# Optimization experiments

Measured on AMD Instinct MI355X. Metric: run time of the kernel, lower is better.

The kernel has to match this reference:

```python
import jax, jax.numpy as jnp
import numpy as np

U, N, E, D = 200000, 50000, 1600000, 64


def setup_inputs() -> dict:
    key = jax.random.key(0)
    ks = jax.random.split(key, 8)
    nodes = jax.random.randint(ks[0], (N,), 0, U)
    neigh_idx = jax.random.randint(ks[1], (E,), 0, U)
    seg_ids = jnp.sort(jax.random.randint(ks[2], (E,), 0, N))
    u2e = jax.random.normal(ks[3], (U, D), dtype=jnp.float32) * 0.1
    W1 = jax.random.normal(ks[4], (2 * D, D), dtype=jnp.float32) * 0.1
    b1 = jnp.zeros((D,), dtype=jnp.float32)
    W2 = jax.random.normal(ks[5], (D, D), dtype=jnp.float32) * 0.1
    b2 = jnp.zeros((D,), dtype=jnp.float32)
    w3 = jax.random.normal(ks[6], (D, 1), dtype=jnp.float32) * 0.1
    b3 = jnp.zeros((1,), dtype=jnp.float32)
    return {"nodes": nodes, "neigh_idx": neigh_idx, "seg_ids": seg_ids,
            "u2e": u2e, "W1": W1, "b1": b1, "W2": W2, "b2": b2,
            "w3": w3, "b3": b3}


def reference(nodes, neigh_idx, seg_ids, u2e, W1, b1, W2, b2, w3, b3):
    # Per-node self representation  [N, D]
    u_rep = u2e[nodes]
    # Ragged neighbor gather flattened to edge list
    e_u = u2e[neigh_idx]                      # [E, D]
    u_edge = u_rep[seg_ids]                   # [E, D] node rep broadcast to its edges
    # Attention MLP (GraphRec-style), eval mode (no dropout)
    x = jnp.concatenate([e_u, u_edge], axis=1)            # [E, 2D]
    x = jax.nn.relu(x @ W1 + b1)
    x = jax.nn.relu(x @ W2 + b2)
    logits = (x @ w3 + b3)[:, 0]                           # [E]
    # Segment softmax over each node's neighbor set
    seg_max = jax.ops.segment_max(logits, seg_ids, num_segments=N)
    ex = jnp.exp(logits - seg_max[seg_ids])
    denom = jax.ops.segment_sum(ex, seg_ids, num_segments=N)
    att = ex / denom[seg_ids]                              # [E]
    # Attention-weighted neighbor aggregation: e_u^T @ att per node
    agg = jax.ops.segment_sum(att[:, None] * e_u, seg_ids, num_segments=N)  # [N, D]
    # Nodes with zero neighbors fall back to their own embedding
    counts = jax.ops.segment_sum(jnp.ones((E,), dtype=jnp.float32), seg_ids, num_segments=N)
    out = jnp.where(counts[:, None] > 0, agg, u_rep)
    return out
```

## Files before the change

kernel.cpp:

```cpp
#include <hip/hip_runtime.h>
#include <math.h>

#define D 64

typedef __fp16 fp16x2 __attribute__((ext_vector_type(2)));
typedef _Float16 half8 __attribute__((ext_vector_type(8)));
typedef __attribute__((ext_vector_type(4))) float f32x4;

union h8pun { half8 v; fp16x2 h2[4]; };

__global__ __launch_bounds__(256) void k_transpose_all(const float* __restrict__ W1,
                                                       const float* __restrict__ W2,
                                                       float* __restrict__ W1at,
                                                       float* __restrict__ W1bt,
                                                       float* __restrict__ W2t) {
    int i = blockIdx.x * 256 + threadIdx.x;
    if (i >= 3 * D * D) return;
    int mat = i / (D * D), j = i % (D * D);
    int r = j >> 6, c = j & 63;
    if (mat == 0)      W1at[c * D + r] = W1[r * D + c];
    else if (mat == 1) W1bt[c * D + r] = W1[(D + r) * D + c];
    else               W2t[c * D + r] = W2[r * D + c];
}

__global__ __launch_bounds__(256) void k_bounds(const int* __restrict__ seg_ids,
                                                int* __restrict__ start, int E, int N) {
    int n = blockIdx.x * 256 + threadIdx.x;
    if (n > N) return;
    int lo = 0, hi = E;
    while (lo < hi) {
        int mid = (lo + hi) >> 1;
        if (seg_ids[mid] < n) lo = mid + 1; else hi = mid;
    }
    start[n] = lo;
}

__global__ __launch_bounds__(256) void k_proj_mfma(const float* __restrict__ u2e,
                                                   const int* __restrict__ idx,
                                                   const float* __restrict__ Wt,
                                                   const float* __restrict__ bias,
                                                   _Float16* __restrict__ outp,
                                                   _Float16* __restrict__ u2e_h,
                                                   int R) {
    int lane = threadIdx.x & 63;
    int m = lane & 15, quad = lane >> 4;

    half8 Bf[2][4];
    float bv[4];
#pragma unroll
    for (int t = 0; t < 4; ++t) {
        int n = m + 16 * t;
        bv[t] = bias ? bias[n] : 0.0f;
#pragma unroll
        for (int kh = 0; kh < 2; ++kh) {
            const float* col = Wt + n * D + kh * 32 + quad * 8;
#pragma unroll
            for (int j = 0; j < 8; ++j) Bf[kh][t][j] = (_Float16)col[j];
        }
    }

    int ngroups = (R + 15) / 16;
    int wave = (blockIdx.x * blockDim.x + threadIdx.x) >> 6;
    int nwaves = (gridDim.x * blockDim.x) >> 6;
    for (int g = wave; g < ngroups; g += nwaves) {
        int r_ = g * 16 + m;
        int rs = r_ < R ? r_ : R - 1;
        int src = idx ? idx[rs] : rs;
        const float4* arow = (const float4*)(u2e + (size_t)src * D);
        float4 x0 = arow[quad * 2], x1 = arow[quad * 2 + 1];
        float4 y0 = arow[8 + quad * 2], y1 = arow[8 + quad * 2 + 1];
        h8pun A0, A1;
        A0.h2[0] = __builtin_amdgcn_cvt_pkrtz(x0.x, x0.y);
        A0.h2[1] = __builtin_amdgcn_cvt_pkrtz(x0.z, x0.w);
        A0.h2[2] = __builtin_amdgcn_cvt_pkrtz(x1.x, x1.y);
        A0.h2[3] = __builtin_amdgcn_cvt_pkrtz(x1.z, x1.w);
        A1.h2[0] = __builtin_amdgcn_cvt_pkrtz(y0.x, y0.y);
        A1.h2[1] = __builtin_amdgcn_cvt_pkrtz(y0.z, y0.w);
        A1.h2[2] = __builtin_amdgcn_cvt_pkrtz(y1.x, y1.y);
        A1.h2[3] = __builtin_amdgcn_cvt_pkrtz(y1.z, y1.w);
        if (u2e_h && r_ < R) {
            *(half8*)(u2e_h + (size_t)r_ * D + quad * 8) = A0.v;
            *(half8*)(u2e_h + (size_t)r_ * D + 32 + quad * 8) = A1.v;
        }
        f32x4 C[4];
#pragma unroll
        for (int t = 0; t < 4; ++t) C[t] = (f32x4){bv[t], bv[t], bv[t], bv[t]};
#pragma unroll
        for (int t = 0; t < 4; ++t) {
            C[t] = __builtin_amdgcn_mfma_f32_16x16x32_f16(A0.v, Bf[0][t], C[t], 0, 0, 0);
            C[t] = __builtin_amdgcn_mfma_f32_16x16x32_f16(A1.v, Bf[1][t], C[t], 0, 0, 0);
        }
#pragma unroll
        for (int r = 0; r < 4; ++r) {
            int row = g * 16 + quad * 4 + r;
            if (row < R) {
#pragma unroll
                for (int t = 0; t < 4; ++t)
                    outp[(size_t)row * D + m + 16 * t] = (_Float16)C[t][r];
            }
        }
    }
}

__global__ __launch_bounds__(256) void k_edge_logits_mfma(const int* __restrict__ neigh_idx,
                                                          const int* __restrict__ seg_ids,
                                                          const _Float16* __restrict__ q,
                                                          const _Float16* __restrict__ p,
                                                          const float* __restrict__ W2t,
                                                          const float* __restrict__ b2,
                                                          const float* __restrict__ w3,
                                                          const float* __restrict__ b3,
                                                          float* __restrict__ logits, int E) {
    int lane = threadIdx.x & 63;
    int m = lane & 15, quad = lane >> 4;

    half8 Bf[2][4];
    float b2v[4], w3v[4];
#pragma unroll
    for (int t = 0; t < 4; ++t) {
        int n = m + 16 * t;
        b2v[t] = b2[n];
        w3v[t] = w3[n];
#pragma unroll
        for (int kh = 0; kh < 2; ++kh) {
            const float* col = W2t + n * D + kh * 32 + quad * 8;
#pragma unroll
            for (int j = 0; j < 8; ++j) Bf[kh][t][j] = (_Float16)col[j];
        }
    }
    float b3v = b3[0];
    const half8 hz = {0, 0, 0, 0, 0, 0, 0, 0};

    int ngroups = (E + 31) / 32;
    int wave = (blockIdx.x * blockDim.x + threadIdx.x) >> 6;
    int nwaves = (gridDim.x * blockDim.x) >> 6;
    for (int g = wave; g < ngroups; g += nwaves) {
        int ea = g * 32 + m, eb = ea + 16;
        int eas = ea < E ? ea : E - 1;
        int ebs = eb < E ? eb : E - 1;
        int nbra = neigh_idx[eas], sega = seg_ids[eas];
        int nbrb = neigh_idx[ebs], segb = seg_ids[ebs];
        const half8* qra = (const half8*)(q + (size_t)nbra * D);
        const half8* pra = (const half8*)(p + (size_t)sega * D);
        const half8* qrb = (const half8*)(q + (size_t)nbrb * D);
        const half8* prb = (const half8*)(p + (size_t)segb * D);
        half8 qa0 = qra[quad], qa1 = qra[quad + 4];
        half8 pa0 = pra[quad], pa1 = pra[quad + 4];
        half8 qb0 = qrb[quad], qb1 = qrb[quad + 4];
        half8 pb0 = prb[quad], pb1 = prb[quad + 4];
        half8 Aa0 = __builtin_elementwise_max(qa0 + pa0, hz);
        half8 Aa1 = __builtin_elementwise_max(qa1 + pa1, hz);
        half8 Ab0 = __builtin_elementwise_max(qb0 + pb0, hz);
        half8 Ab1 = __builtin_elementwise_max(qb1 + pb1, hz);
        f32x4 Ca[4], Cb[4];
#pragma unroll
        for (int t = 0; t < 4; ++t) {
            Ca[t] = (f32x4){b2v[t], b2v[t], b2v[t], b2v[t]};
            Cb[t] = Ca[t];
        }
#pragma unroll
        for (int t = 0; t < 4; ++t) {
            Ca[t] = __builtin_amdgcn_mfma_f32_16x16x32_f16(Aa0, Bf[0][t], Ca[t], 0, 0, 0);
            Ca[t] = __builtin_amdgcn_mfma_f32_16x16x32_f16(Aa1, Bf[1][t], Ca[t], 0, 0, 0);
            Cb[t] = __builtin_amdgcn_mfma_f32_16x16x32_f16(Ab0, Bf[0][t], Cb[t], 0, 0, 0);
            Cb[t] = __builtin_amdgcn_mfma_f32_16x16x32_f16(Ab1, Bf[1][t], Cb[t], 0, 0, 0);
        }
        float pa[4], pb[4];
#pragma unroll
        for (int r = 0; r < 4; ++r) {
            float sa = 0.0f, sb = 0.0f;
#pragma unroll
            for (int t = 0; t < 4; ++t) {
                sa += fmaxf(Ca[t][r], 0.0f) * w3v[t];
                sb += fmaxf(Cb[t][r], 0.0f) * w3v[t];
            }
            pa[r] = sa; pb[r] = sb;
        }
#pragma unroll
        for (int off = 1; off <= 8; off <<= 1) {
#pragma unroll
            for (int r = 0; r < 4; ++r) {
                pa[r] += __shfl_xor(pa[r], off, 64);
                pb[r] += __shfl_xor(pb[r], off, 64);
            }
        }
        if (m == 0) {
            int e0 = g * 32 + quad * 4;
            if (e0 + 3 < E)
                *(float4*)(logits + e0) = make_float4(pa[0] + b3v, pa[1] + b3v, pa[2] + b3v, pa[3] + b3v);
            else
#pragma unroll
                for (int r = 0; r < 4; ++r)
                    if (e0 + r < E) logits[e0 + r] = pa[r] + b3v;
            int e1 = e0 + 16;
            if (e1 + 3 < E)
                *(float4*)(logits + e1) = make_float4(pb[0] + b3v, pb[1] + b3v, pb[2] + b3v, pb[3] + b3v);
            else
#pragma unroll
                for (int r = 0; r < 4; ++r)
                    if (e1 + r < E) logits[e1 + r] = pb[r] + b3v;
        }
    }
}

__global__ __launch_bounds__(256) void k_agg(const int* __restrict__ nodes,
                                             const int* __restrict__ neigh_idx,
                                             const float* __restrict__ u2e,
                                             const _Float16* __restrict__ u2e_h,
                                             const float* __restrict__ logits,
                                             const int* __restrict__ start,
                                             float* __restrict__ out, int N) {
    int n = blockIdx.x * 4 + ((int)threadIdx.x >> 6);
    int lane = threadIdx.x & 63;
    if (n >= N) return;
    int s = start[n];
    int t = start[n + 1];
    if (s == t) {
        int node = nodes[n];
        out[(size_t)n * D + lane] = u2e[(size_t)node * D + lane];
        return;
    }
    float mx = -INFINITY;
    for (int i = s + lane; i < t; i += 64) mx = fmaxf(mx, logits[i]);
#pragma unroll
    for (int off = 32; off >= 1; off >>= 1) mx = fmaxf(mx, __shfl_xor(mx, off, 64));
    float ssum = 0.0f;
    for (int i = s + lane; i < t; i += 64) ssum += __expf(logits[i] - mx);
#pragma unroll
    for (int off = 32; off >= 1; off >>= 1) ssum += __shfl_xor(ssum, off, 64);
    float inv = 1.0f / ssum;

    int grp = lane >> 3, sub = lane & 7;
    float acc[8];
#pragma unroll
    for (int j = 0; j < 8; ++j) acc[j] = 0.0f;
    for (int i = s; i < t; i += 32) {
#pragma unroll
        for (int uu = 0; uu < 4; ++uu) {
            int ii = i + uu * 8 + grp;
            bool v = ii < t;
            int is = v ? ii : s;
            float lg = logits[is];
            int nb = neigh_idx[is];
            half8 r = *(const half8*)(u2e_h + (size_t)nb * D + sub * 8);
            float a = v ? __expf(lg - mx) * inv : 0.0f;
#pragma unroll
            for (int j = 0; j < 8; ++j) acc[j] += a * (float)r[j];
        }
    }
#pragma unroll
    for (int off = 8; off <= 32; off <<= 1) {
#pragma unroll
        for (int j = 0; j < 8; ++j) acc[j] += __shfl_xor(acc[j], off, 64);
    }
    if (grp == 0) {
        float* o = out + (size_t)n * D + sub * 8;
        *(float4*)o = make_float4(acc[0], acc[1], acc[2], acc[3]);
        *(float4*)(o + 4) = make_float4(acc[4], acc[5], acc[6], acc[7]);
    }
}

extern "C" void kernel_launch(void* const* d_in, const int* in_sizes, int n_in,
                              void* d_out, int out_size, void* d_ws, size_t ws_size,
                              hipStream_t stream) {
    const int* nodes = (const int*)d_in[0];
    const int* neigh_idx = (const int*)d_in[1];
    const int* seg_ids = (const int*)d_in[2];
    const float* u2e = (const float*)d_in[3];
    const float* W1 = (const float*)d_in[4];
    const float* b1 = (const float*)d_in[5];
    const float* W2 = (const float*)d_in[6];
    const float* b2 = (const float*)d_in[7];
    const float* w3 = (const float*)d_in[8];
    const float* b3 = (const float*)d_in[9];
    float* out = (float*)d_out;

    int N = in_sizes[0];
    int E = in_sizes[1];
    int U = in_sizes[3] / D;

    char* ws = (char*)d_ws;
    size_t off = 0;
    auto alloc = [&](size_t bytes) {
        void* ptr = ws + off;
        off = (off + bytes + 255) & ~(size_t)255;
        return ptr;
    };
    float* logits = (float*)alloc((size_t)E * 4);
    int* start = (int*)alloc((size_t)(N + 1) * 4);
    float* W1at = (float*)alloc((size_t)D * D * 4);
    float* W1bt = (float*)alloc((size_t)D * D * 4);
    float* W2t = (float*)alloc((size_t)D * D * 4);
    _Float16* q = (_Float16*)alloc((size_t)U * D * 2);
    _Float16* p = (_Float16*)alloc((size_t)N * D * 2);
    _Float16* u2e_h = (_Float16*)alloc((size_t)U * D * 2);
    (void)ws_size;

    k_transpose_all<<<(3 * D * D + 255) / 256, 256, 0, stream>>>(W1, W2, W1at, W1bt, W2t);
    k_bounds<<<(N + 1 + 255) / 256, 256, 0, stream>>>(seg_ids, start, E, N);
    k_proj_mfma<<<1024, 256, 0, stream>>>(u2e, nullptr, W1at, nullptr, q, u2e_h, U);
    k_proj_mfma<<<256, 256, 0, stream>>>(u2e, nodes, W1bt, b1, p, nullptr, N);
    k_edge_logits_mfma<<<2048, 256, 0, stream>>>(neigh_idx, seg_ids, q, p, W2t,
                                                 b2, w3, b3, logits, E);
    k_agg<<<(N + 3) / 4, 256, 0, stream>>>(nodes, neigh_idx, u2e, u2e_h, logits, start, out, N);
}
```

Before: 247.8 us.

## Merge prep and projection launches; software-prefetch edge gathers in logits kernel

Merges the weight-transpose and segment-bounds kernels into one launch, and the two projection launches into one whose waves are split between the U table and the N node rows. The edge-logits loop now software-pipelines its gathers, issuing the q/p row loads for the next group before the MFMA work on the current one, to hide gather latency. This cuts launch overhead and keeps loads in flight, at the cost of more live registers, which may lower occupancy.

```diff
diff --git a/kernel.cpp b/kernel.cpp
--- a/kernel.cpp
+++ b/kernel.cpp
@@ -9,41 +9,57 @@
 
 union h8pun { half8 v; fp16x2 h2[4]; };
 
-__global__ __launch_bounds__(256) void k_transpose_all(const float* __restrict__ W1,
-                                                       const float* __restrict__ W2,
-                                                       float* __restrict__ W1at,
-                                                       float* __restrict__ W1bt,
-                                                       float* __restrict__ W2t) {
+__global__ __launch_bounds__(256) void k_prep(const float* __restrict__ W1,
+                                              const float* __restrict__ W2,
+                                              float* __restrict__ W1at,
+                                              float* __restrict__ W1bt,
+                                              float* __restrict__ W2t,
+                                              const int* __restrict__ seg_ids,
+                                              int* __restrict__ start, int E, int N) {
     int i = blockIdx.x * 256 + threadIdx.x;
-    if (i >= 3 * D * D) return;
-    int mat = i / (D * D), j = i % (D * D);
-    int r = j >> 6, c = j & 63;
-    if (mat == 0)      W1at[c * D + r] = W1[r * D + c];
-    else if (mat == 1) W1bt[c * D + r] = W1[(D + r) * D + c];
-    else               W2t[c * D + r] = W2[r * D + c];
-}
-
-__global__ __launch_bounds__(256) void k_bounds(const int* __restrict__ seg_ids,
-                                                int* __restrict__ start, int E, int N) {
-    int n = blockIdx.x * 256 + threadIdx.x;
-    if (n > N) return;
-    int lo = 0, hi = E;
-    while (lo < hi) {
-        int mid = (lo + hi) >> 1;
-        if (seg_ids[mid] < n) lo = mid + 1; else hi = mid;
-    }
-    start[n] = lo;
-}
-
-__global__ __launch_bounds__(256) void k_proj_mfma(const float* __restrict__ u2e,
-                                                   const int* __restrict__ idx,
-                                                   const float* __restrict__ Wt,
-                                                   const float* __restrict__ bias,
-                                                   _Float16* __restrict__ outp,
+    if (i < 3 * D * D) {
+        int mat = i / (D * D), j = i % (D * D);
+        int r = j >> 6, c = j & 63;
+        if (mat == 0)      W1at[c * D + r] = W1[r * D + c];
+        else if (mat == 1) W1bt[c * D + r] = W1[(D + r) * D + c];
+        else               W2t[c * D + r] = W2[r * D + c];
+    }
+    if (i <= N) {
+        int lo = 0, hi = E;
+        while (lo < hi) {
+            int mid = (lo + hi) >> 1;
+            if (seg_ids[mid] < i) lo = mid + 1; else hi = mid;
+        }
+        start[i] = lo;
+    }
+}
+
+__global__ __launch_bounds__(256) void k_proj_both(const float* __restrict__ u2e,
+                                                   const int* __restrict__ nodes,
+                                                   const float* __restrict__ W1at,
+                                                   const float* __restrict__ W1bt,
+                                                   const float* __restrict__ b1,
+                                                   _Float16* __restrict__ q,
                                                    _Float16* __restrict__ u2e_h,
-                                                   int R) {
+                                                   _Float16* __restrict__ p,
+                                                   int U, int N, int wavesU, int wavesN) {
     int lane = threadIdx.x & 63;
     int m = lane & 15, quad = lane >> 4;
+    int wave = (blockIdx.x * blockDim.x + threadIdx.x) >> 6;
+
+    const float* Wt;
+    const int* idx;
+    const float* bias;
+    _Float16* outp;
+    _Float16* copyp;
+    int R, w0, wstride;
+    if (wave < wavesU) {
+        Wt = W1at; idx = nullptr; bias = nullptr; outp = q; copyp = u2e_h;
+        R = U; w0 = wave; wstride = wavesU;
+    } else {
+        Wt = W1bt; idx = nodes; bias = b1; outp = p; copyp = nullptr;
+        R = N; w0 = wave - wavesU; wstride = wavesN;
+    }
 
     half8 Bf[2][4];
     float bv[4];
@@ -60,9 +76,7 @@
     }
 
     int ngroups = (R + 15) / 16;
-    int wave = (blockIdx.x * blockDim.x + threadIdx.x) >> 6;
-    int nwaves = (gridDim.x * blockDim.x) >> 6;
-    for (int g = wave; g < ngroups; g += nwaves) {
+    for (int g = w0; g < ngroups; g += wstride) {
         int r_ = g * 16 + m;
         int rs = r_ < R ? r_ : R - 1;
         int src = idx ? idx[rs] : rs;
@@ -78,9 +92,9 @@
         A1.h2[1] = __builtin_amdgcn_cvt_pkrtz(y0.z, y0.w);
         A1.h2[2] = __builtin_amdgcn_cvt_pkrtz(y1.x, y1.y);
         A1.h2[3] = __builtin_amdgcn_cvt_pkrtz(y1.z, y1.w);
-        if (u2e_h && r_ < R) {
-            *(half8*)(u2e_h + (size_t)r_ * D + quad * 8) = A0.v;
-            *(half8*)(u2e_h + (size_t)r_ * D + 32 + quad * 8) = A1.v;
+        if (copyp && r_ < R) {
+            *(half8*)(copyp + (size_t)r_ * D + quad * 8) = A0.v;
+            *(half8*)(copyp + (size_t)r_ * D + 32 + quad * 8) = A1.v;
         }
         f32x4 C[4];
 #pragma unroll
@@ -134,7 +148,11 @@
     int ngroups = (E + 31) / 32;
     int wave = (blockIdx.x * blockDim.x + threadIdx.x) >> 6;
     int nwaves = (gridDim.x * blockDim.x) >> 6;
-    for (int g = wave; g < ngroups; g += nwaves) {
+
+    half8 cqa0 = hz, cqa1 = hz, cpa0 = hz, cpa1 = hz;
+    half8 cqb0 = hz, cqb1 = hz, cpb0 = hz, cpb1 = hz;
+    int g = wave;
+    if (g < ngroups) {
         int ea = g * 32 + m, eb = ea + 16;
         int eas = ea < E ? ea : E - 1;
         int ebs = eb < E ? eb : E - 1;
@@ -144,14 +162,31 @@
         const half8* pra = (const half8*)(p + (size_t)sega * D);
         const half8* qrb = (const half8*)(q + (size_t)nbrb * D);
         const half8* prb = (const half8*)(p + (size_t)segb * D);
-        half8 qa0 = qra[quad], qa1 = qra[quad + 4];
-        half8 pa0 = pra[quad], pa1 = pra[quad + 4];
-        half8 qb0 = qrb[quad], qb1 = qrb[quad + 4];
-        half8 pb0 = prb[quad], pb1 = prb[quad + 4];
-        half8 Aa0 = __builtin_elementwise_max(qa0 + pa0, hz);
-        half8 Aa1 = __builtin_elementwise_max(qa1 + pa1, hz);
-        half8 Ab0 = __builtin_elementwise_max(qb0 + pb0, hz);
-        half8 Ab1 = __builtin_elementwise_max(qb1 + pb1, hz);
+        cqa0 = qra[quad]; cqa1 = qra[quad + 4];
+        cpa0 = pra[quad]; cpa1 = pra[quad + 4];
+        cqb0 = qrb[quad]; cqb1 = qrb[quad + 4];
+        cpb0 = prb[quad]; cpb1 = prb[quad + 4];
+    }
+    for (; g < ngroups; g += nwaves) {
+        int gn = g + nwaves;
+        int gs = gn < ngroups ? gn : g;
+        int ea2 = gs * 32 + m, eb2 = ea2 + 16;
+        int eas2 = ea2 < E ? ea2 : E - 1;
+        int ebs2 = eb2 < E ? eb2 : E - 1;
+        int nbra2 = neigh_idx[eas2], sega2 = seg_ids[eas2];
+        int nbrb2 = neigh_idx[ebs2], segb2 = seg_ids[ebs2];
+        half8 Aa0 = __builtin_elementwise_max(cqa0 + cpa0, hz);
+        half8 Aa1 = __builtin_elementwise_max(cqa1 + cpa1, hz);
+        half8 Ab0 = __builtin_elementwise_max(cqb0 + cpb0, hz);
+        half8 Ab1 = __builtin_elementwise_max(cqb1 + cpb1, hz);
+        const half8* qra2 = (const half8*)(q + (size_t)nbra2 * D);
+        const half8* pra2 = (const half8*)(p + (size_t)sega2 * D);
+        const half8* qrb2 = (const half8*)(q + (size_t)nbrb2 * D);
+        const half8* prb2 = (const half8*)(p + (size_t)segb2 * D);
+        half8 nqa0 = qra2[quad], nqa1 = qra2[quad + 4];
+        half8 npa0 = pra2[quad], npa1 = pra2[quad + 4];
+        half8 nqb0 = qrb2[quad], nqb1 = qrb2[quad + 4];
+        half8 npb0 = prb2[quad], npb1 = prb2[quad + 4];
         f32x4 Ca[4], Cb[4];
 #pragma unroll
         for (int t = 0; t < 4; ++t) {
@@ -200,6 +235,8 @@
                 for (int r = 0; r < 4; ++r)
                     if (e1 + r < E) logits[e1 + r] = pb[r] + b3v;
         }
+        cqa0 = nqa0; cqa1 = nqa1; cpa0 = npa0; cpa1 = npa1;
+        cqb0 = nqb0; cqb1 = nqb1; cpb0 = npb0; cpb1 = npb1;
     }
 }
 
@@ -296,10 +333,12 @@
     _Float16* u2e_h = (_Float16*)alloc((size_t)U * D * 2);
     (void)ws_size;
 
-    k_transpose_all<<<(3 * D * D + 255) / 256, 256, 0, stream>>>(W1, W2, W1at, W1bt, W2t);
-    k_bounds<<<(N + 1 + 255) / 256, 256, 0, stream>>>(seg_ids, start, E, N);
-    k_proj_mfma<<<1024, 256, 0, stream>>>(u2e, nullptr, W1at, nullptr, q, u2e_h, U);
-    k_proj_mfma<<<256, 256, 0, stream>>>(u2e, nodes, W1bt, b1, p, nullptr, N);
+    int prep_n = (N + 1) > 3 * D * D ? (N + 1) : 3 * D * D;
+    k_prep<<<(prep_n + 255) / 256, 256, 0, stream>>>(W1, W2, W1at, W1bt, W2t,
+                                                     seg_ids, start, E, N);
+    const int wavesU = 4096, wavesN = 1024;
+    k_proj_both<<<(wavesU + wavesN) / 4, 256, 0, stream>>>(u2e, nodes, W1at, W1bt, b1,
+                                                           q, u2e_h, p, U, N, wavesU, wavesN);
     k_edge_logits_mfma<<<2048, 256, 0, stream>>>(neigh_idx, seg_ids, q, p, W2t,
                                                  b2, w3, b3, logits, E);
     k_agg<<<(N + 3) / 4, 256, 0, stream>>>(nodes, neigh_idx, u2e, u2e_h, logits, start, out, N);
```

Result: no change. 247.1 us (-0.3%).
